# Kernel optimization log

Measured on AMD Instinct MI355X. Metric: run time of the kernel, lower is better.

## Reference

```python
import jax, jax.numpy as jnp
from jax import lax
import numpy as np

T = 4096
VOCAB = 32000
EMBD = 192
HIDDEN = 512


def setup_inputs() -> dict:
    key = jax.random.key(0)
    ks = jax.random.split(key, 8)
    s = 0.05  # init scale
    return {
        "X": jax.random.randint(ks[0], (T,), 0, VOCAB, dtype=jnp.int64 if jax.config.jax_enable_x64 else jnp.int32),
        "emb": jax.random.normal(ks[1], (VOCAB, EMBD), jnp.float32) * s,
        "W_in": jax.random.normal(ks[2], (EMBD, HIDDEN), jnp.float32) * s,
        "b_in": jnp.zeros((HIDDEN,), jnp.float32),
        "W_f": jax.random.normal(ks[3], (2 * HIDDEN, HIDDEN), jnp.float32) * s,
        "b_f": jnp.zeros((HIDDEN,), jnp.float32),
        "W_is": jax.random.normal(ks[4], (2 * HIDDEN, HIDDEN), jnp.float32) * s,
        "b_is": jnp.zeros((HIDDEN,), jnp.float32),
        "W_it": jax.random.normal(ks[5], (2 * HIDDEN, HIDDEN), jnp.float32) * s,
        "b_it": jnp.zeros((HIDDEN,), jnp.float32),
        "W_o": jax.random.normal(ks[6], (2 * HIDDEN, HIDDEN), jnp.float32) * s,
        "b_o": jnp.zeros((HIDDEN,), jnp.float32),
        "W_head": jax.random.normal(ks[7], (HIDDEN, VOCAB), jnp.float32) * s,
        "b_head": jnp.zeros((VOCAB,), jnp.float32),
    }


def reference(X, emb, W_in, b_in, W_f, b_f, W_is, b_is, W_it, b_it, W_o, b_o, W_head, b_head):
    # Embedding lookup + input projection: [T, EMBD] -> [T, HIDDEN]
    x_seq = emb[X] @ W_in + b_in

    hidden = W_f.shape[1]

    def lstm_cell(carry, x):
        c, h = carry
        hx = jnp.concatenate([h, x])                      # [2H]
        f = jax.nn.sigmoid(hx @ W_f + b_f)                # forget gate
        i_sig = jax.nn.sigmoid(hx @ W_is + b_is)          # input gate (sigmoid)
        i_tanh = jnp.tanh(hx @ W_it + b_it)               # input gate (tanh)
        c = c * f + i_sig * i_tanh
        o = jax.nn.sigmoid(hx @ W_o + b_o)                # output gate
        h = jnp.tanh(c) * o
        return (c, h), h

    init = (jnp.zeros((hidden,), x_seq.dtype), jnp.zeros((hidden,), x_seq.dtype))
    _, hs = lax.scan(lstm_cell, init, x_seq)              # hs: [T, H]
    logits = hs @ W_head + b_head                         # [T, VOCAB]
    return logits
```

## Files before the change

### kernel.cpp

```cpp
#include <hip/hip_runtime.h>
#include <hip/hip_bf16.h>

#define T_SEQ  4096
#define VOCAB  32000
#define EMBD   192
#define HID    512

typedef __attribute__((ext_vector_type(8))) short  short8;
typedef __attribute__((ext_vector_type(4))) float  f32x4;

__global__ __launch_bounds__(256) void k_embed(const int* __restrict__ X,
                                               const float* __restrict__ emb,
                                               const float* __restrict__ W_in,
                                               const float* __restrict__ b_in,
                                               float* __restrict__ xseq) {
    const int n  = blockIdx.x * 256 + threadIdx.x;
    const int m0 = blockIdx.y * 8;
    int xm[8];
#pragma unroll
    for (int i = 0; i < 8; ++i) xm[i] = X[m0 + i];
    float acc[8];
    const float bv = b_in[n];
#pragma unroll
    for (int i = 0; i < 8; ++i) acc[i] = bv;
    for (int k = 0; k < EMBD; ++k) {
        const float wv = W_in[k * HID + n];
#pragma unroll
        for (int i = 0; i < 8; ++i)
            acc[i] = fmaf(emb[(size_t)xm[i] * EMBD + k], wv, acc[i]);
    }
#pragma unroll
    for (int i = 0; i < 8; ++i) xseq[(size_t)(m0 + i) * HID + n] = acc[i];
}

__global__ __launch_bounds__(256) void k_gx(const float* __restrict__ xseq,
                                            const float* __restrict__ Wf, const float* __restrict__ Wis,
                                            const float* __restrict__ Wit, const float* __restrict__ Wo,
                                            const float* __restrict__ bf_, const float* __restrict__ bis,
                                            const float* __restrict__ bit_, const float* __restrict__ bo,
                                            float* __restrict__ Gx) {
    __shared__ float Asm[64 * 17];
    __shared__ float Bsm[16 * 64];
    const int tid = threadIdx.x;
    const int n0 = blockIdx.x * 64;
    const int m0 = blockIdx.y * 64;
    const int g  = n0 >> 9;
    const int j0 = n0 & 511;
    const float* W    = (g == 0) ? Wf  : (g == 1) ? Wis : (g == 2) ? Wit : Wo;
    const float* bias = (g == 0) ? bf_ : (g == 1) ? bis : (g == 2) ? bit_ : bo;
    const int tx = tid & 15, ty = tid >> 4;
    float acc[4][4] = {};
    const int r  = tid >> 2, c4 = (tid & 3) * 4;
    const int kr = tid >> 4, nq = (tid & 15) * 4;
    for (int kk = 0; kk < HID; kk += 16) {
        float4 av = *(const float4*)&xseq[(size_t)(m0 + r) * HID + kk + c4];
        Asm[r * 17 + c4 + 0] = av.x; Asm[r * 17 + c4 + 1] = av.y;
        Asm[r * 17 + c4 + 2] = av.z; Asm[r * 17 + c4 + 3] = av.w;
        float4 bv = *(const float4*)&W[(size_t)(HID + kk + kr) * HID + j0 + nq];
        *(float4*)&Bsm[kr * 64 + nq] = bv;
        __syncthreads();
#pragma unroll
        for (int k = 0; k < 16; ++k) {
            float4 b4 = *(const float4*)&Bsm[k * 64 + tx * 4];
            float a0 = Asm[(ty * 4 + 0) * 17 + k];
            float a1 = Asm[(ty * 4 + 1) * 17 + k];
            float a2 = Asm[(ty * 4 + 2) * 17 + k];
            float a3 = Asm[(ty * 4 + 3) * 17 + k];
            acc[0][0] += a0 * b4.x; acc[0][1] += a0 * b4.y; acc[0][2] += a0 * b4.z; acc[0][3] += a0 * b4.w;
            acc[1][0] += a1 * b4.x; acc[1][1] += a1 * b4.y; acc[1][2] += a1 * b4.z; acc[1][3] += a1 * b4.w;
            acc[2][0] += a2 * b4.x; acc[2][1] += a2 * b4.y; acc[2][2] += a2 * b4.z; acc[2][3] += a2 * b4.w;
            acc[3][0] += a3 * b4.x; acc[3][1] += a3 * b4.y; acc[3][2] += a3 * b4.z; acc[3][3] += a3 * b4.w;
        }
        __syncthreads();
    }
    float4 bia = *(const float4*)&bias[j0 + tx * 4];
#pragma unroll
    for (int i = 0; i < 4; ++i) {
        float4 o;
        o.x = acc[i][0] + bia.x; o.y = acc[i][1] + bia.y;
        o.z = acc[i][2] + bia.z; o.w = acc[i][3] + bia.w;
        *(float4*)&Gx[(size_t)(m0 + ty * 4 + i) * 2048 + n0 + tx * 4] = o;
    }
}

__global__ __launch_bounds__(256) void k_twh(const float* __restrict__ Wh,
                                             __hip_bfloat16* __restrict__ WT) {
    __shared__ float tile[32][33];
    const int tid = threadIdx.x;
    const int n0 = blockIdx.x * 32, k0 = blockIdx.y * 32;
    const int tx = tid & 31, ty = tid >> 5;
#pragma unroll
    for (int i = 0; i < 4; ++i)
        tile[ty + 8 * i][tx] = Wh[(size_t)(k0 + ty + 8 * i) * VOCAB + n0 + tx];
    __syncthreads();
#pragma unroll
    for (int i = 0; i < 4; ++i) {
        const int n = ty + 8 * i;
        WT[(size_t)(n0 + n) * HID + k0 + tx] = __float2bfloat16(tile[tx][n]);
    }
}

__global__ __launch_bounds__(256, 1) void k_lstm(const float* __restrict__ Gx,
                                                 const float* __restrict__ Wf, const float* __restrict__ Wis,
                                                 const float* __restrict__ Wit, const float* __restrict__ Wo,
                                                 __hip_bfloat16* __restrict__ hs_out,
                                                 unsigned long long* h_seq ) {
    const int w   = blockIdx.x;
    const int tid = threadIdx.x;
    const int g   = tid >> 6;
    const int l   = tid & 63;
    const int u   = l >> 3;
    const int s   = l & 7;
    const int jcol = w * 8 + u;
    const float* Wg = (g == 0) ? Wf : (g == 1) ? Wis : (g == 2) ? Wit : Wo;

    float wreg[64];
#pragma unroll
    for (int d = 0; d < 8; ++d)
#pragma unroll
        for (int c = 0; c < 8; ++c)
            wreg[d * 8 + c] = Wg[(size_t)(8 * s + c + 64 * d) * HID + jcol];

    __shared__ float h_lds[512];
    __shared__ float zsc[32];
    float creg = 0.f;

#pragma unroll 1
    for (int t = 0; t < T_SEQ; ++t) {
        float gx = 0.f;
        if (s == 0) gx = Gx[(size_t)t * 2048 + g * 512 + jcol];

        if (t > 0) {
            unsigned long long* hb = h_seq + (size_t)((t - 1) & 1) * 512;
            const unsigned tag = (unsigned)t;
            unsigned long long v0, v1;
            for (;;) {
                v0 = __hip_atomic_load(&hb[2 * tid],     __ATOMIC_RELAXED, __HIP_MEMORY_SCOPE_AGENT);
                v1 = __hip_atomic_load(&hb[2 * tid + 1], __ATOMIC_RELAXED, __HIP_MEMORY_SCOPE_AGENT);
                if ((unsigned)(v0 >> 32) == tag && (unsigned)(v1 >> 32) == tag) break;
            }
            h_lds[2 * tid]     = __uint_as_float((unsigned)v0);
            h_lds[2 * tid + 1] = __uint_as_float((unsigned)v1);
        } else {
            h_lds[2 * tid] = 0.f;
            h_lds[2 * tid + 1] = 0.f;
        }
        __syncthreads();

        float acc = 0.f;
#pragma unroll
        for (int d = 0; d < 8; ++d) {
            const float4* hp = (const float4*)&h_lds[8 * s + 64 * d];
            float4 ha = hp[0], hb4 = hp[1];
            acc += wreg[d * 8 + 0] * ha.x + wreg[d * 8 + 1] * ha.y +
                   wreg[d * 8 + 2] * ha.z + wreg[d * 8 + 3] * ha.w +
                   wreg[d * 8 + 4] * hb4.x + wreg[d * 8 + 5] * hb4.y +
                   wreg[d * 8 + 6] * hb4.z + wreg[d * 8 + 7] * hb4.w;
        }
        acc += __shfl_xor(acc, 1);
        acc += __shfl_xor(acc, 2);
        acc += __shfl_xor(acc, 4);
        if (s == 0) zsc[g * 8 + u] = acc + gx;
        __syncthreads();

        if (tid < 8) {
            const float zf = zsc[tid], zi = zsc[8 + tid], zt = zsc[16 + tid], zo = zsc[24 + tid];
            const float f  = 1.f / (1.f + __expf(-zf));
            const float ii = 1.f / (1.f + __expf(-zi));
            const float it = tanhf(zt);
            const float o  = 1.f / (1.f + __expf(-zo));
            creg = creg * f + ii * it;
            const float hv = tanhf(creg) * o;
            hs_out[(size_t)t * HID + w * 8 + tid] = __float2bfloat16(hv);
            const unsigned long long pk =
                ((unsigned long long)(unsigned)(t + 1) << 32) | (unsigned long long)__float_as_uint(hv);
            __hip_atomic_store(&h_seq[(size_t)(t & 1) * 512 + w * 8 + tid], pk,
                               __ATOMIC_RELAXED, __HIP_MEMORY_SCOPE_AGENT);
        }
        __syncthreads();
    }
}

__global__ __launch_bounds__(256) void k_head(const __hip_bfloat16* __restrict__ hsb,
                                              const __hip_bfloat16* __restrict__ WT,
                                              const float* __restrict__ b_head,
                                              float* __restrict__ out) {
    __shared__ unsigned short Al[128 * 40];
    __shared__ unsigned short Bl[128 * 40];
    const int tid = threadIdx.x;
    const int n0 = blockIdx.x * 128;
    const int m0 = blockIdx.y * 128;
    const int wv = tid >> 6;
    const int l  = tid & 63;
    const int m_off = (wv & 1) * 64;
    const int n_off = (wv >> 1) * 64;
    const int lr = l & 15;
    const int lq = l >> 4;
    const unsigned short* hsu = (const unsigned short*)hsb;
    const unsigned short* wtu = (const unsigned short*)WT;
    const int sr = tid >> 1;
    const int sh = (tid & 1) * 16;

    f32x4 acc[4][4];
#pragma unroll
    for (int i = 0; i < 4; ++i)
#pragma unroll
        for (int j = 0; j < 4; ++j)
            acc[i][j] = (f32x4){0.f, 0.f, 0.f, 0.f};

    for (int kk = 0; kk < HID; kk += 32) {
        {
            const short8* ga = (const short8*)&hsu[(size_t)(m0 + sr) * HID + kk + sh];
            short8 a0 = ga[0], a1 = ga[1];
            *(short8*)&Al[sr * 40 + sh]     = a0;
            *(short8*)&Al[sr * 40 + sh + 8] = a1;
            const short8* gb = (const short8*)&wtu[(size_t)(n0 + sr) * HID + kk + sh];
            short8 b0 = gb[0], b1 = gb[1];
            *(short8*)&Bl[sr * 40 + sh]     = b0;
            *(short8*)&Bl[sr * 40 + sh + 8] = b1;
        }
        __syncthreads();
        short8 af[4], bfr[4];
#pragma unroll
        for (int i = 0; i < 4; ++i)
            af[i] = *(const short8*)&Al[(m_off + i * 16 + lr) * 40 + lq * 8];
#pragma unroll
        for (int j = 0; j < 4; ++j)
            bfr[j] = *(const short8*)&Bl[(n_off + j * 16 + lr) * 40 + lq * 8];
#pragma unroll
        for (int i = 0; i < 4; ++i)
#pragma unroll
            for (int j = 0; j < 4; ++j)
                acc[i][j] = __builtin_amdgcn_mfma_f32_16x16x32_bf16(af[i], bfr[j], acc[i][j], 0, 0, 0);
        __syncthreads();
    }
#pragma unroll
    for (int j = 0; j < 4; ++j) {
        const int col = n0 + n_off + j * 16 + lr;
        const float bh = b_head[col];
#pragma unroll
        for (int i = 0; i < 4; ++i) {
            const int rowb = m0 + m_off + i * 16 + lq * 4;
#pragma unroll
            for (int r = 0; r < 4; ++r)
                out[(size_t)(rowb + r) * VOCAB + col] = acc[i][j][r] + bh;
        }
    }
}

extern "C" void kernel_launch(void* const* d_in, const int* in_sizes, int n_in,
                              void* d_out, int out_size, void* d_ws, size_t ws_size,
                              hipStream_t stream) {
    const int*   X      = (const int*)  d_in[0];
    const float* emb    = (const float*)d_in[1];
    const float* W_in   = (const float*)d_in[2];
    const float* b_in   = (const float*)d_in[3];
    const float* W_f    = (const float*)d_in[4];
    const float* b_f    = (const float*)d_in[5];
    const float* W_is   = (const float*)d_in[6];
    const float* b_is   = (const float*)d_in[7];
    const float* W_it   = (const float*)d_in[8];
    const float* b_it   = (const float*)d_in[9];
    const float* W_o    = (const float*)d_in[10];
    const float* b_o    = (const float*)d_in[11];
    const float* W_head = (const float*)d_in[12];
    const float* b_head = (const float*)d_in[13];
    float* out = (float*)d_out;

    char* ws = (char*)d_ws;
    float*              xseq  = (float*)(ws);
    float*              Gx    = (float*)(ws + ((size_t)8  << 20));
    __hip_bfloat16*     hsb   = (__hip_bfloat16*)(ws + ((size_t)40 << 20));
    __hip_bfloat16*     WT    = (__hip_bfloat16*)(ws + ((size_t)44 << 20));
    unsigned long long* h_seq = (unsigned long long*)(ws + ((size_t)76 << 20));

    k_embed<<<dim3(2, 512),    256, 0, stream>>>(X, emb, W_in, b_in, xseq);
    k_gx   <<<dim3(32, 64),    256, 0, stream>>>(xseq, W_f, W_is, W_it, W_o,
                                                 b_f, b_is, b_it, b_o, Gx);
    k_twh  <<<dim3(1000, 16),  256, 0, stream>>>(W_head, WT);
    k_lstm <<<dim3(64),        256, 0, stream>>>(Gx, W_f, W_is, W_it, W_o, hsb, h_seq);
    k_head <<<dim3(250, 32),   256, 0, stream>>>(hsb, WT, b_head, out);
}
```

Baseline: 7.916 ms.

## Regroup LSTM gates per wavefront to drop two block barriers per step

Remaps threads so each wavefront holds all four gates for two hidden units. Gate values can then be gathered with intra-wave shuffles instead of a shared-memory scratch and an extra barrier. The LDS h buffer is double-buffered, which removes the trailing barrier each timestep, and every lane computes the cell redundantly. Sigmoid and tanh are switched to fast rcp/exp forms and the dot product uses four independent FMA chains, trading some numerical accuracy for a shorter serial critical path.

```diff
diff --git a/kernel.cpp b/kernel.cpp
--- a/kernel.cpp
+++ b/kernel.cpp
@@ -100,6 +100,13 @@
     }
 }
 
+__device__ __forceinline__ float fsig(float x) {
+    return __builtin_amdgcn_rcpf(1.f + __expf(-x));
+}
+__device__ __forceinline__ float ftanh(float x) {
+    return fmaf(-2.f, __builtin_amdgcn_rcpf(__expf(2.f * x) + 1.f), 1.f);
+}
+
 __global__ __launch_bounds__(256, 1) void k_lstm(const float* __restrict__ Gx,
                                                  const float* __restrict__ Wf, const float* __restrict__ Wis,
                                                  const float* __restrict__ Wit, const float* __restrict__ Wo,
@@ -107,12 +114,13 @@
                                                  unsigned long long* h_seq ) {
     const int w   = blockIdx.x;
     const int tid = threadIdx.x;
-    const int g   = tid >> 6;
+    const int v   = tid >> 6;
     const int l   = tid & 63;
-    const int u   = l >> 3;
+    const int u   = l >> 5;
+    const int gg  = (l >> 3) & 3;
     const int s   = l & 7;
-    const int jcol = w * 8 + u;
-    const float* Wg = (g == 0) ? Wf : (g == 1) ? Wis : (g == 2) ? Wit : Wo;
+    const int jcol = w * 8 + 2 * v + u;
+    const float* Wg = (gg == 0) ? Wf : (gg == 1) ? Wis : (gg == 2) ? Wit : Wo;
 
     float wreg[64];
 #pragma unroll
@@ -121,15 +129,15 @@
         for (int c = 0; c < 8; ++c)
             wreg[d * 8 + c] = Wg[(size_t)(8 * s + c + 64 * d) * HID + jcol];
 
-    __shared__ float h_lds[512];
-    __shared__ float zsc[32];
+    __shared__ float h_lds[2][512];
     float creg = 0.f;
+    const int gbase = l & 32;
 
 #pragma unroll 1
     for (int t = 0; t < T_SEQ; ++t) {
-        float gx = 0.f;
-        if (s == 0) gx = Gx[(size_t)t * 2048 + g * 512 + jcol];
-
+        const float gx = Gx[(size_t)t * 2048 + gg * 512 + jcol];
+
+        float* hl = h_lds[t & 1];
         if (t > 0) {
             unsigned long long* hb = h_seq + (size_t)((t - 1) & 1) * 512;
             const unsigned tag = (unsigned)t;
@@ -137,47 +145,55 @@
             for (;;) {
                 v0 = __hip_atomic_load(&hb[2 * tid],     __ATOMIC_RELAXED, __HIP_MEMORY_SCOPE_AGENT);
                 v1 = __hip_atomic_load(&hb[2 * tid + 1], __ATOMIC_RELAXED, __HIP_MEMORY_SCOPE_AGENT);
-                if ((unsigned)(v0 >> 32) == tag && (unsigned)(v1 >> 32) == tag) break;
+                if (((unsigned)(v0 >> 32) == tag) & ((unsigned)(v1 >> 32) == tag)) break;
             }
-            h_lds[2 * tid]     = __uint_as_float((unsigned)v0);
-            h_lds[2 * tid + 1] = __uint_as_float((unsigned)v1);
+            hl[2 * tid]     = __uint_as_float((unsigned)v0);
+            hl[2 * tid + 1] = __uint_as_float((unsigned)v1);
         } else {
-            h_lds[2 * tid] = 0.f;
-            h_lds[2 * tid + 1] = 0.f;
-        }
-        __syncthreads();
-
-        float acc = 0.f;
+            hl[2 * tid]     = 0.f;
+            hl[2 * tid + 1] = 0.f;
+        }
+        __syncthreads();
+
+        float a0 = 0.f, a1 = 0.f, a2 = 0.f, a3 = 0.f;
 #pragma unroll
         for (int d = 0; d < 8; ++d) {
-            const float4* hp = (const float4*)&h_lds[8 * s + 64 * d];
+            const float4* hp = (const float4*)&hl[8 * s + 64 * d];
             float4 ha = hp[0], hb4 = hp[1];
-            acc += wreg[d * 8 + 0] * ha.x + wreg[d * 8 + 1] * ha.y +
-                   wreg[d * 8 + 2] * ha.z + wreg[d * 8 + 3] * ha.w +
-                   wreg[d * 8 + 4] * hb4.x + wreg[d * 8 + 5] * hb4.y +
-                   wreg[d * 8 + 6] * hb4.z + wreg[d * 8 + 7] * hb4.w;
-        }
-        acc += __shfl_xor(acc, 1);
-        acc += __shfl_xor(acc, 2);
-        acc += __shfl_xor(acc, 4);
-        if (s == 0) zsc[g * 8 + u] = acc + gx;
-        __syncthreads();
-
-        if (tid < 8) {
-            const float zf = zsc[tid], zi = zsc[8 + tid], zt = zsc[16 + tid], zo = zsc[24 + tid];
-            const float f  = 1.f / (1.f + __expf(-zf));
-            const float ii = 1.f / (1.f + __expf(-zi));
-            const float it = tanhf(zt);
-            const float o  = 1.f / (1.f + __expf(-zo));
-            creg = creg * f + ii * it;
-            const float hv = tanhf(creg) * o;
-            hs_out[(size_t)t * HID + w * 8 + tid] = __float2bfloat16(hv);
+            a0 = fmaf(wreg[d * 8 + 0], ha.x,  a0);
+            a1 = fmaf(wreg[d * 8 + 1], ha.y,  a1);
+            a2 = fmaf(wreg[d * 8 + 2], ha.z,  a2);
+            a3 = fmaf(wreg[d * 8 + 3], ha.w,  a3);
+            a0 = fmaf(wreg[d * 8 + 4], hb4.x, a0);
+            a1 = fmaf(wreg[d * 8 + 5], hb4.y, a1);
+            a2 = fmaf(wreg[d * 8 + 6], hb4.z, a2);
+            a3 = fmaf(wreg[d * 8 + 7], hb4.w, a3);
+        }
+        float z = (a0 + a1) + (a2 + a3);
+        z += __shfl_xor(z, 1);
+        z += __shfl_xor(z, 2);
+        z += __shfl_xor(z, 4);
+        z += gx;
+
+        const float zf = __shfl(z, gbase + 0);
+        const float zi = __shfl(z, gbase + 8);
+        const float zt = __shfl(z, gbase + 16);
+        const float zo = __shfl(z, gbase + 24);
+
+        const float f  = fsig(zf);
+        const float ii = fsig(zi);
+        const float it = ftanh(zt);
+        const float o  = fsig(zo);
+        creg = creg * f + ii * it;
+        const float hv = ftanh(creg) * o;
+
+        if ((l & 31) == 0) {
+            hs_out[(size_t)t * HID + jcol] = __float2bfloat16(hv);
             const unsigned long long pk =
                 ((unsigned long long)(unsigned)(t + 1) << 32) | (unsigned long long)__float_as_uint(hv);
-            __hip_atomic_store(&h_seq[(size_t)(t & 1) * 512 + w * 8 + tid], pk,
+            __hip_atomic_store(&h_seq[(size_t)(t & 1) * 512 + jcol], pk,
                                __ATOMIC_RELAXED, __HIP_MEMORY_SCOPE_AGENT);
         }
-        __syncthreads();
     }
 }
 
```

Result: slower. 9.436 ms (+19.2%).
